# Performance work log

Hardware: AMD Instinct MI355X
Metric: run time of the kernel (lower is better)

The kernel has to match this reference:

```python
import jax, jax.numpy as jnp
import numpy as np

B, S, C = 64, 512, 512   # batch, subseq_length, in_features
H, D = 4, 128            # n_heads, hidden_features (H*D == C)
LN_EPS = 1e-5


def setup_inputs() -> dict:
    key = jax.random.key(0)
    k_h, k_w, k_b = jax.random.split(key, 3)
    h = jax.random.normal(k_h, (B, S, C), dtype=jnp.float32)
    # stacked per-head Linear weights, stored as [H, in, hid] for x @ W
    W = jax.random.normal(k_w, (H, C, D), dtype=jnp.float32) * (1.0 / np.sqrt(C))
    b = jax.random.normal(k_b, (H, D), dtype=jnp.float32) * 0.01
    adj = jnp.ones((S, S), dtype=jnp.float32)
    gamma = jnp.ones((C,), dtype=jnp.float32)
    beta = jnp.zeros((C,), dtype=jnp.float32)
    return {"t": 0, "h": h, "W": W, "b": b, "adj": adj, "gamma": gamma, "beta": beta}


def reference(t, h, W, b, adj, gamma, beta):
    # per-head projection: [H, B, S, D]
    hp = jnp.einsum("bsc,hcd->hbsd", h, W) + b[:, None, None, :]
    # raw scores, multiplicative adjacency mask (non-standard: mask BEFORE softmax by multiply)
    scores = jnp.einsum("hbsd,hbtd->hbst", hp, hp) * adj
    attn = jax.nn.softmax(scores, axis=-1)
    out = jnp.einsum("hbst,hbtd->hbsd", attn, hp)
    # concat heads along feature dim -> [B, S, H*D] == [B, S, C]
    out = jnp.transpose(out, (1, 2, 0, 3)).reshape(h.shape[0], h.shape[1], -1)
    # LayerNorm over last dim
    mu = jnp.mean(out, axis=-1, keepdims=True)
    var = jnp.mean(jnp.square(out - mu), axis=-1, keepdims=True)
    out = (out - mu) * jax.lax.rsqrt(var + LN_EPS) * gamma + beta
    # GELU (exact erf form, matching torch nn.GELU default)
    return jax.nn.gelu(out, approximate=False)
```

## Files before the change

kernel.cpp:

```cpp
#include <hip/hip_runtime.h>
#include <stdint.h>


typedef float  f32x4   __attribute__((ext_vector_type(4)));
typedef short  bf16x8  __attribute__((ext_vector_type(8)));
typedef unsigned short ushort8 __attribute__((ext_vector_type(8)));
typedef unsigned int   uint2v  __attribute__((ext_vector_type(2)));

#define GLD16(src, dst)                                                        \
  __builtin_amdgcn_global_load_lds(                                            \
      (const __attribute__((address_space(1))) void*)(src),                    \
      (__attribute__((address_space(3))) void*)(dst), 16, 0, 0)

__device__ __forceinline__ unsigned short f32_to_bf16(float x) {
  union { float f; unsigned int u; } v; v.f = x;
  unsigned int r = v.u + 0x7FFFu + ((v.u >> 16) & 1u);
  return (unsigned short)(r >> 16);
}
__device__ __forceinline__ float bf16_to_f32(unsigned int h) {
  union { float f; unsigned int u; } v; v.u = h << 16;
  return v.f;
}
__device__ __forceinline__ f32x4 mfma16(bf16x8 a, bf16x8 b, f32x4 c) {
  return __builtin_amdgcn_mfma_f32_16x16x32_bf16(a, b, c, 0, 0, 0);
}
__device__ __forceinline__ float bperm_f(int srcLane, float v) {
  return __int_as_float(__builtin_amdgcn_ds_bpermute(srcLane << 2, __float_as_int(v)));
}
__device__ __forceinline__ uint2v tr_read(const unsigned short* p) {
  uint2v r;
  asm volatile("ds_read_b64_tr_b16 %0, %1"
               : "=v"(r)
               : "v"((const __attribute__((address_space(3))) void*)p)
               : "memory");
  return r;
}

__global__ __launch_bounds__(256) void cast_split_Wt(
    const float* __restrict__ W, unsigned short* __restrict__ whi,
    unsigned short* __restrict__ wlo) {
  int o = blockIdx.x * 256 + threadIdx.x;
  int hd = o >> 16;
  int rem = o & 65535;
  int d = rem >> 9;
  int c = rem & 511;
  float v = W[((size_t)(hd * 512 + c)) * 128 + d];
  unsigned short h0 = f32_to_bf16(v);
  whi[o] = h0;
  wlo[o] = f32_to_bf16(v - bf16_to_f32(h0));
}

__global__ __launch_bounds__(256) void cast_adj(
    const float* __restrict__ src, unsigned short* __restrict__ dst) {
  size_t i = ((size_t)blockIdx.x * 256 + threadIdx.x) * 8;
  f32x4 a = *(const f32x4*)(src + i);
  f32x4 b = *(const f32x4*)(src + i + 4);
  ushort8 o;
#pragma unroll
  for (int e = 0; e < 4; ++e) {
    o[e] = f32_to_bf16(a[e]);
    o[4 + e] = f32_to_bf16(b[e]);
  }
  *(ushort8*)(dst + i) = o;
}

__global__ __launch_bounds__(256, 2) void proj_gemm(
    const float* __restrict__ hsrc,
    const unsigned short* __restrict__ whi, const unsigned short* __restrict__ wlo,
    const float* __restrict__ bias, unsigned short* __restrict__ hp_hi,
    unsigned short* __restrict__ hp_lo) {
  int bid = blockIdx.x;
  int swz = (bid & 7) * 128 + (bid >> 3);
  int nt = swz & 3, mt = swz >> 2;
  int m0 = mt * 128, n0 = nt * 128;

  __shared__ alignas(16) unsigned short Ah[4096], Al[4096], Bh[4096], Bl[4096];

  int tid = threadIdx.x, wv = tid >> 6, lane = tid & 63;
  int l15 = lane & 15, l4 = lane >> 4;
  int wr = wv >> 1, wc = wv & 1;
  int arow = tid >> 3;
  int acol = (tid & 7) * 4;

  f32x4 acc[4][4];
#pragma unroll
  for (int a = 0; a < 4; ++a)
#pragma unroll
    for (int b = 0; b < 4; ++b) acc[a][b] = (f32x4){0.f, 0.f, 0.f, 0.f};

  for (int ks = 0; ks < 16; ++ks) {
    int k0 = ks * 32;
    for (int i = wv; i < 16; i += 4) {
      int grp = i >> 3, j = i & 7;
      int row = j * 16 + (lane >> 2);
      int off = (lane & 3) * 16;
      int sw = ((row >> 1) & 3) << 4;
      const unsigned short* sb = grp ? wlo : whi;
      unsigned short* db = grp ? Bl : Bh;
      GLD16((const char*)sb + ((size_t)(nt * 128 + row) * 512 + k0) * 2 + (off ^ sw),
            db + j * 512);
    }
#pragma unroll
    for (int j = 0; j < 4; ++j) {
      int r = j * 32 + arow;
      f32x4 x = *(const f32x4*)(hsrc + (size_t)(m0 + r) * 512 + k0 + acol);
      unsigned ua = __float_as_uint(x[0]), ub = __float_as_uint(x[1]);
      unsigned uc = __float_as_uint(x[2]), ud = __float_as_uint(x[3]);
      uint2 ph, pl;
      ph.x = (ua >> 16) | (ub & 0xFFFF0000u);
      ph.y = (uc >> 16) | (ud & 0xFFFF0000u);
      float ra = x[0] - __uint_as_float(ua & 0xFFFF0000u);
      float rb = x[1] - __uint_as_float(ub & 0xFFFF0000u);
      float rc = x[2] - __uint_as_float(uc & 0xFFFF0000u);
      float rd = x[3] - __uint_as_float(ud & 0xFFFF0000u);
      pl.x = (__float_as_uint(ra) >> 16) | (__float_as_uint(rb) & 0xFFFF0000u);
      pl.y = (__float_as_uint(rc) >> 16) | (__float_as_uint(rd) & 0xFFFF0000u);
      int boff = r * 64 + ((acol * 2) ^ (((r >> 1) & 3) << 4));
      *(uint2*)((char*)Ah + boff) = ph;
      *(uint2*)((char*)Al + boff) = pl;
    }
    __syncthreads();

    bf16x8 fah[4], fal[4], fbh[4], fbl[4];
#pragma unroll
    for (int f = 0; f < 4; ++f) {
      int mr = wr * 64 + f * 16 + l15;
      int aadr = mr * 64 + ((16 * l4) ^ (((mr >> 1) & 3) << 4));
      fah[f] = *(const bf16x8*)((const char*)Ah + aadr);
      fal[f] = *(const bf16x8*)((const char*)Al + aadr);
      int nr = wc * 64 + f * 16 + l15;
      int badr = nr * 64 + ((16 * l4) ^ (((nr >> 1) & 3) << 4));
      fbh[f] = *(const bf16x8*)((const char*)Bh + badr);
      fbl[f] = *(const bf16x8*)((const char*)Bl + badr);
    }
#pragma unroll
    for (int a = 0; a < 4; ++a)
#pragma unroll
      for (int b = 0; b < 4; ++b) {
        acc[a][b] = mfma16(fah[a], fbh[b], acc[a][b]);
        acc[a][b] = mfma16(fah[a], fbl[b], acc[a][b]);
        acc[a][b] = mfma16(fal[a], fbh[b], acc[a][b]);
      }
    __syncthreads();
  }

#pragma unroll
  for (int a = 0; a < 4; ++a) {
    __syncthreads();
#pragma unroll
    for (int b = 0; b < 4; ++b) {
      int cloc = wc * 64 + b * 16 + l15;
      float bv = bias[n0 + cloc];
#pragma unroll
      for (int r = 0; r < 4; ++r) {
        int rloc = wr * 16 + 4 * l4 + r;
        float v = acc[a][b][r] + bv;
        unsigned short hh = f32_to_bf16(v);
        Ah[rloc * 128 + cloc] = hh;
        Al[rloc * 128 + cloc] = f32_to_bf16(v - bf16_to_f32(hh));
      }
    }
    __syncthreads();
    int rr = tid >> 3, c16 = (tid & 7) * 16;
    int mg = m0 + (rr >> 4) * 64 + a * 16 + (rr & 15);
    bf16x8 vh0 = *(const bf16x8*)(Ah + rr * 128 + c16);
    bf16x8 vh1 = *(const bf16x8*)(Ah + rr * 128 + c16 + 8);
    bf16x8 vl0 = *(const bf16x8*)(Al + rr * 128 + c16);
    bf16x8 vl1 = *(const bf16x8*)(Al + rr * 128 + c16 + 8);
    *(bf16x8*)(hp_hi + (size_t)mg * 512 + n0 + c16) = vh0;
    *(bf16x8*)(hp_hi + (size_t)mg * 512 + n0 + c16 + 8) = vh1;
    *(bf16x8*)(hp_lo + (size_t)mg * 512 + n0 + c16) = vl0;
    *(bf16x8*)(hp_lo + (size_t)mg * 512 + n0 + c16 + 8) = vl1;
  }
}

__global__ __launch_bounds__(256, 3) void attn_kernel(
    const unsigned short* __restrict__ hp_hi, const unsigned short* __restrict__ hp_lo,
    const unsigned short* __restrict__ adjb, unsigned short* __restrict__ ob) {
  int bid = blockIdx.x;
  int swz = (bid & 7) * 256 + (bid >> 3);
  int qt = swz & 7;
  int hd = (swz >> 3) & 3;
  int bb = swz >> 5;
  int q0 = qt * 64;

  __shared__ alignas(16) unsigned short SM[24576];

  int tid = threadIdx.x, w = tid >> 6, lane = tid & 63;
  int l15 = lane & 15, l4 = lane >> 4;
  int qg = q0 + w * 16 + l15;

  bf16x8 qh[4], ql[4];
  {
    size_t base = ((size_t)bb * 512 + qg) * 512 + hd * 128 + 8 * l4;
#pragma unroll
    for (int ds = 0; ds < 4; ++ds) {
      qh[ds] = *(const bf16x8*)(hp_hi + base + ds * 32);
      ql[ds] = *(const bf16x8*)(hp_lo + base + ds * 32);
    }
  }

  f32x4 o[8];
#pragma unroll
  for (int vf = 0; vf < 8; ++vf) o[vf] = (f32x4){0.f, 0.f, 0.f, 0.f};
  float m_run = -3.0e38f, l_run = 0.f;

  const unsigned short* ssb = (w & 2) ? hp_lo : hp_hi;
  int sdst = (w & 2) ? 4096 : 0;
  int sdbase = (w & 1) * 4;
  int skv = lane >> 1, sdh = lane & 1;

  {
    size_t rowb = ((size_t)(bb * 512 + skv)) * 1024 + hd * 256 + sdh * 16;
#pragma unroll
    for (int s2 = 0; s2 < 4; ++s2) {
      int sd = sdbase + s2;
      GLD16((const char*)ssb + rowb + sd * 32, SM + sdst + sd * 512);
    }
  }
  asm volatile("s_waitcnt vmcnt(0)" ::: "memory");
  __syncthreads();

  for (int t = 0; t < 16; ++t) {
    int kv0 = t * 32;
    const unsigned short* Kb = SM + ((t & 1) << 13);
    const unsigned short* Khi = Kb;
    const unsigned short* Klo = Kb + 4096;

    if (t < 15) {
      unsigned short* Nb = SM + (((t + 1) & 1) << 13) + sdst;
      size_t rowb = ((size_t)(bb * 512 + kv0 + 32 + skv)) * 1024 + hd * 256 + sdh * 16;
#pragma unroll
      for (int s2 = 0; s2 < 4; ++s2) {
        int sd = sdbase + s2;
        GLD16((const char*)ssb + rowb + sd * 32, Nb + sd * 512);
      }
    }
    uint2 ua0 = *(const uint2*)(adjb + (size_t)qg * 512 + kv0 + 4 * l4);
    uint2 ua1 = *(const uint2*)(adjb + (size_t)qg * 512 + kv0 + 16 + 4 * l4);
    f32x4 av0, av1;
    av0[0] = bf16_to_f32(ua0.x & 0xFFFFu); av0[1] = bf16_to_f32(ua0.x >> 16);
    av0[2] = bf16_to_f32(ua0.y & 0xFFFFu); av0[3] = bf16_to_f32(ua0.y >> 16);
    av1[0] = bf16_to_f32(ua1.x & 0xFFFFu); av1[1] = bf16_to_f32(ua1.x >> 16);
    av1[2] = bf16_to_f32(ua1.y & 0xFFFFu); av1[3] = bf16_to_f32(ua1.y >> 16);

    f32x4 sc0 = {0.f, 0.f, 0.f, 0.f}, sc1 = {0.f, 0.f, 0.f, 0.f};
#pragma unroll
    for (int ds = 0; ds < 4; ++ds) {
      int boff = (2 * ds + (l4 >> 1)) * 1024 + 16 * (l4 & 1);
      int a0 = boff + l15 * 32;
      int a1 = boff + (16 + l15) * 32;
      bf16x8 kh0 = *(const bf16x8*)((const char*)Khi + a0);
      bf16x8 kl0 = *(const bf16x8*)((const char*)Klo + a0);
      bf16x8 kh1 = *(const bf16x8*)((const char*)Khi + a1);
      bf16x8 kl1 = *(const bf16x8*)((const char*)Klo + a1);
      sc0 = mfma16(kh0, qh[ds], sc0); sc1 = mfma16(kh1, qh[ds], sc1);
      sc0 = mfma16(kh0, ql[ds], sc0); sc1 = mfma16(kh1, ql[ds], sc1);
      sc0 = mfma16(kl0, qh[ds], sc0); sc1 = mfma16(kl1, qh[ds], sc1);
    }

    float p0[4], p1[4];
    float tm = -3.0e38f;
#pragma unroll
    for (int r = 0; r < 4; ++r) {
      p0[r] = sc0[r] * av0[r];
      p1[r] = sc1[r] * av1[r];
      tm = fmaxf(tm, fmaxf(p0[r], p1[r]));
    }
    tm = fmaxf(tm, __shfl_xor(tm, 16));
    tm = fmaxf(tm, __shfl_xor(tm, 32));
    if (__any(tm > m_run + 8.0f)) {
      float mn = fmaxf(m_run, tm);
      float scl = __expf(m_run - mn);
      m_run = mn;
      l_run *= scl;
      f32x4 s4;
#pragma unroll
      for (int r = 0; r < 4; ++r) s4[r] = bperm_f(4 * l4 + r, scl);
#pragma unroll
      for (int vf = 0; vf < 8; ++vf)
#pragma unroll
        for (int r = 0; r < 4; ++r) o[vf][r] *= s4[r];
    }
    float ps = 0.f;
#pragma unroll
    for (int r = 0; r < 4; ++r) {
      p0[r] = __expf(p0[r] - m_run); ps += p0[r];
      p1[r] = __expf(p1[r] - m_run); ps += p1[r];
    }
    ps += __shfl_xor(ps, 16);
    ps += __shfl_xor(ps, 32);
    l_run += ps;

    union PU { bf16x8 v; unsigned u[4]; } pah;
#pragma unroll
    for (int i = 0; i < 4; ++i) {
      float fa = (i < 2) ? p0[2 * i] : p1[2 * (i - 2)];
      float fb = (i < 2) ? p0[2 * i + 1] : p1[2 * (i - 2) + 1];
      pah.u[i] = (__float_as_uint(fa) >> 16) |
                 (__float_as_uint(fb) & 0xFFFF0000u);
    }

    const unsigned short* trb = Khi + lane * 4;
    union VU { bf16x8 v; uint2v u2[2]; } vh[8];
#pragma unroll
    for (int vf = 0; vf < 8; ++vf) {
      vh[vf].u2[0] = tr_read(trb + vf * 512);
      vh[vf].u2[1] = tr_read(trb + vf * 512 + 256);
    }
    asm volatile("s_waitcnt lgkmcnt(0)" ::: "memory");
    __builtin_amdgcn_sched_barrier(0);
#pragma unroll
    for (int vf = 0; vf < 8; ++vf)
      o[vf] = mfma16(pah.v, vh[vf].v, o[vf]);
    asm volatile("s_waitcnt vmcnt(0) lgkmcnt(0)" ::: "memory");
    __syncthreads();
  }

  float rinv = 1.0f / l_run;
  f32x4 r4;
#pragma unroll
  for (int r = 0; r < 4; ++r) r4[r] = bperm_f(4 * l4 + r, rinv);
  float* wbase = (float*)SM + w * 2048;
#pragma unroll
  for (int vf = 0; vf < 8; ++vf)
#pragma unroll
    for (int r = 0; r < 4; ++r)
      wbase[(4 * l4 + r) * 128 + vf * 16 + l15] = o[vf][r] * r4[r];
  __syncthreads();
#pragma unroll
  for (int p = 0; p < 4; ++p) {
    int row = p * 4 + l4;
    f32x4 v0 = *(const f32x4*)(wbase + row * 128 + l15 * 8);
    f32x4 v1 = *(const f32x4*)(wbase + row * 128 + l15 * 8 + 4);
    ushort8 o8;
#pragma unroll
    for (int e = 0; e < 4; ++e) {
      o8[e] = f32_to_bf16(v0[e]);
      o8[4 + e] = f32_to_bf16(v1[e]);
    }
    size_t mg = (size_t)bb * 512 + q0 + w * 16 + row;
    *(ushort8*)(ob + mg * 512 + hd * 128 + l15 * 8) = o8;
  }
}

__global__ __launch_bounds__(256) void ln_gelu_kernel(
    const unsigned short* __restrict__ in, float* __restrict__ outp,
    const float* __restrict__ gamma, const float* __restrict__ beta) {
  int w = threadIdx.x >> 6, lane = threadIdx.x & 63;
  size_t row = (size_t)blockIdx.x * 4 + w;
  ushort8 v = *(const ushort8*)(in + row * 512 + lane * 8);
  float x[8];
#pragma unroll
  for (int e = 0; e < 8; ++e) x[e] = bf16_to_f32((unsigned int)(unsigned short)v[e]);
  float s = 0.f;
#pragma unroll
  for (int e = 0; e < 8; ++e) s += x[e];
#pragma unroll
  for (int off = 32; off >= 1; off >>= 1) s += __shfl_xor(s, off);
  float mu = s * (1.0f / 512.0f);
  float vs = 0.f;
#pragma unroll
  for (int e = 0; e < 8; ++e) {
    float d = x[e] - mu; vs += d * d;
  }
#pragma unroll
  for (int off = 32; off >= 1; off >>= 1) vs += __shfl_xor(vs, off);
  float rs = rsqrtf(vs * (1.0f / 512.0f) + 1e-5f);
  f32x4 g0 = *(const f32x4*)(gamma + lane * 8);
  f32x4 g1 = *(const f32x4*)(gamma + lane * 8 + 4);
  f32x4 b0 = *(const f32x4*)(beta + lane * 8);
  f32x4 b1 = *(const f32x4*)(beta + lane * 8 + 4);
  f32x4 y0, y1;
#pragma unroll
  for (int e = 0; e < 4; ++e) {
    float y = (x[e] - mu) * rs * g0[e] + b0[e];
    y0[e] = 0.5f * y * (1.0f + erff(y * 0.70710678118654752f));
    float z = (x[4 + e] - mu) * rs * g1[e] + b1[e];
    y1[e] = 0.5f * z * (1.0f + erff(z * 0.70710678118654752f));
  }
  float* p = outp + row * 512 + lane * 8;
  *(f32x4*)p = y0;
  *(f32x4*)(p + 4) = y1;
}

extern "C" void kernel_launch(void* const* d_in, const int* in_sizes, int n_in,
                              void* d_out, int out_size, void* d_ws, size_t ws_size,
                              hipStream_t stream) {
  const float* h     = (const float*)d_in[1];
  const float* W     = (const float*)d_in[2];
  const float* bias  = (const float*)d_in[3];
  const float* adj   = (const float*)d_in[4];
  const float* gamma = (const float*)d_in[5];
  const float* beta  = (const float*)d_in[6];
  float* out = (float*)d_out;

  unsigned short* ws = (unsigned short*)d_ws;
  unsigned short* adj_bf = ws;
  unsigned short* ob     = ws + 16777216;
  unsigned short* hp_hi  = ws + 33554432;
  unsigned short* hp_lo  = ws + 50331648;
  unsigned short* Wt_hi  = ws + 67108864;
  unsigned short* Wt_lo  = ws + 67371008;

  cast_split_Wt<<<1024, 256, 0, stream>>>(W, Wt_hi, Wt_lo);
  cast_adj<<<128, 256, 0, stream>>>(adj, adj_bf);
  proj_gemm<<<1024, 256, 0, stream>>>(h, Wt_hi, Wt_lo, bias, hp_hi, hp_lo);
  attn_kernel<<<2048, 256, 0, stream>>>(hp_hi, hp_lo, adj_bf, ob);
  ln_gelu_kernel<<<8192, 256, 0, stream>>>(ob, out, gamma, beta);
}
```

Before: 194.0 us.

## Process two query fragments per wave to reuse K/V tiles in attention

Each attention block now covers 128 query rows instead of 64, and each wave handles two 16-row query fragments that share the same K/V LDS loads and transposed V reads. The aim is to halve K/V global-to-LDS traffic and LDS reads per query, giving more MFMA work per load. In exchange it doubles per-wave accumulators and registers, lowers occupancy (launch bounds 3 to 2), and halves the grid to 1024 blocks, which may leave fewer waves to hide latency.

```diff
diff --git a/kernel.cpp b/kernel.cpp
--- a/kernel.cpp
+++ b/kernel.cpp
@@ -174,36 +174,40 @@
   }
 }
 
-__global__ __launch_bounds__(256, 3) void attn_kernel(
+__global__ __launch_bounds__(256, 2) void attn_kernel(
     const unsigned short* __restrict__ hp_hi, const unsigned short* __restrict__ hp_lo,
     const unsigned short* __restrict__ adjb, unsigned short* __restrict__ ob) {
   int bid = blockIdx.x;
-  int swz = (bid & 7) * 256 + (bid >> 3);
-  int qt = swz & 7;
-  int hd = (swz >> 3) & 3;
-  int bb = swz >> 5;
-  int q0 = qt * 64;
-
-  __shared__ alignas(16) unsigned short SM[24576];
+  int swz = (bid & 7) * 128 + (bid >> 3);
+  int qt = swz & 3;
+  int hd = (swz >> 2) & 3;
+  int bb = swz >> 4;
+  int q0 = qt * 128;
+
+  __shared__ alignas(16) unsigned short SM[28672];
 
   int tid = threadIdx.x, w = tid >> 6, lane = tid & 63;
   int l15 = lane & 15, l4 = lane >> 4;
-  int qg = q0 + w * 16 + l15;
-
-  bf16x8 qh[4], ql[4];
-  {
-    size_t base = ((size_t)bb * 512 + qg) * 512 + hd * 128 + 8 * l4;
+  int qgb = q0 + w * 32 + l15;
+
+  bf16x8 qh[2][4], ql[2][4];
+#pragma unroll
+  for (int nf = 0; nf < 2; ++nf) {
+    size_t base = ((size_t)bb * 512 + qgb + nf * 16) * 512 + hd * 128 + 8 * l4;
 #pragma unroll
     for (int ds = 0; ds < 4; ++ds) {
-      qh[ds] = *(const bf16x8*)(hp_hi + base + ds * 32);
-      ql[ds] = *(const bf16x8*)(hp_lo + base + ds * 32);
-    }
-  }
-
-  f32x4 o[8];
-#pragma unroll
-  for (int vf = 0; vf < 8; ++vf) o[vf] = (f32x4){0.f, 0.f, 0.f, 0.f};
-  float m_run = -3.0e38f, l_run = 0.f;
+      qh[nf][ds] = *(const bf16x8*)(hp_hi + base + ds * 32);
+      ql[nf][ds] = *(const bf16x8*)(hp_lo + base + ds * 32);
+    }
+  }
+
+  f32x4 o[2][8];
+#pragma unroll
+  for (int nf = 0; nf < 2; ++nf)
+#pragma unroll
+    for (int vf = 0; vf < 8; ++vf) o[nf][vf] = (f32x4){0.f, 0.f, 0.f, 0.f};
+  float m_run[2] = {-3.0e38f, -3.0e38f};
+  float l_run[2] = {0.f, 0.f};
 
   const unsigned short* ssb = (w & 2) ? hp_lo : hp_hi;
   int sdst = (w & 2) ? 4096 : 0;
@@ -236,15 +240,19 @@
         GLD16((const char*)ssb + rowb + sd * 32, Nb + sd * 512);
       }
     }
-    uint2 ua0 = *(const uint2*)(adjb + (size_t)qg * 512 + kv0 + 4 * l4);
-    uint2 ua1 = *(const uint2*)(adjb + (size_t)qg * 512 + kv0 + 16 + 4 * l4);
-    f32x4 av0, av1;
-    av0[0] = bf16_to_f32(ua0.x & 0xFFFFu); av0[1] = bf16_to_f32(ua0.x >> 16);
-    av0[2] = bf16_to_f32(ua0.y & 0xFFFFu); av0[3] = bf16_to_f32(ua0.y >> 16);
-    av1[0] = bf16_to_f32(ua1.x & 0xFFFFu); av1[1] = bf16_to_f32(ua1.x >> 16);
-    av1[2] = bf16_to_f32(ua1.y & 0xFFFFu); av1[3] = bf16_to_f32(ua1.y >> 16);
-
-    f32x4 sc0 = {0.f, 0.f, 0.f, 0.f}, sc1 = {0.f, 0.f, 0.f, 0.f};
+    uint2 ua[2][2];
+#pragma unroll
+    for (int nf = 0; nf < 2; ++nf) {
+      const unsigned short* ab = adjb + (size_t)(qgb + nf * 16) * 512 + kv0;
+      ua[nf][0] = *(const uint2*)(ab + 4 * l4);
+      ua[nf][1] = *(const uint2*)(ab + 16 + 4 * l4);
+    }
+
+    f32x4 sc[2][2];
+#pragma unroll
+    for (int nf = 0; nf < 2; ++nf)
+#pragma unroll
+      for (int mf = 0; mf < 2; ++mf) sc[nf][mf] = (f32x4){0.f, 0.f, 0.f, 0.f};
 #pragma unroll
     for (int ds = 0; ds < 4; ++ds) {
       int boff = (2 * ds + (l4 >> 1)) * 1024 + 16 * (l4 & 1);
@@ -254,51 +262,68 @@
       bf16x8 kl0 = *(const bf16x8*)((const char*)Klo + a0);
       bf16x8 kh1 = *(const bf16x8*)((const char*)Khi + a1);
       bf16x8 kl1 = *(const bf16x8*)((const char*)Klo + a1);
-      sc0 = mfma16(kh0, qh[ds], sc0); sc1 = mfma16(kh1, qh[ds], sc1);
-      sc0 = mfma16(kh0, ql[ds], sc0); sc1 = mfma16(kh1, ql[ds], sc1);
-      sc0 = mfma16(kl0, qh[ds], sc0); sc1 = mfma16(kl1, qh[ds], sc1);
-    }
-
-    float p0[4], p1[4];
-    float tm = -3.0e38f;
-#pragma unroll
-    for (int r = 0; r < 4; ++r) {
-      p0[r] = sc0[r] * av0[r];
-      p1[r] = sc1[r] * av1[r];
-      tm = fmaxf(tm, fmaxf(p0[r], p1[r]));
-    }
-    tm = fmaxf(tm, __shfl_xor(tm, 16));
-    tm = fmaxf(tm, __shfl_xor(tm, 32));
-    if (__any(tm > m_run + 8.0f)) {
-      float mn = fmaxf(m_run, tm);
-      float scl = __expf(m_run - mn);
-      m_run = mn;
-      l_run *= scl;
-      f32x4 s4;
-#pragma unroll
-      for (int r = 0; r < 4; ++r) s4[r] = bperm_f(4 * l4 + r, scl);
-#pragma unroll
-      for (int vf = 0; vf < 8; ++vf)
-#pragma unroll
-        for (int r = 0; r < 4; ++r) o[vf][r] *= s4[r];
-    }
-    float ps = 0.f;
-#pragma unroll
-    for (int r = 0; r < 4; ++r) {
-      p0[r] = __expf(p0[r] - m_run); ps += p0[r];
-      p1[r] = __expf(p1[r] - m_run); ps += p1[r];
-    }
-    ps += __shfl_xor(ps, 16);
-    ps += __shfl_xor(ps, 32);
-    l_run += ps;
-
-    union PU { bf16x8 v; unsigned u[4]; } pah;
-#pragma unroll
-    for (int i = 0; i < 4; ++i) {
-      float fa = (i < 2) ? p0[2 * i] : p1[2 * (i - 2)];
-      float fb = (i < 2) ? p0[2 * i + 1] : p1[2 * (i - 2) + 1];
-      pah.u[i] = (__float_as_uint(fa) >> 16) |
-                 (__float_as_uint(fb) & 0xFFFF0000u);
+#pragma unroll
+      for (int nf = 0; nf < 2; ++nf) {
+        sc[nf][0] = mfma16(kh0, qh[nf][ds], sc[nf][0]);
+        sc[nf][1] = mfma16(kh1, qh[nf][ds], sc[nf][1]);
+        sc[nf][0] = mfma16(kh0, ql[nf][ds], sc[nf][0]);
+        sc[nf][1] = mfma16(kh1, ql[nf][ds], sc[nf][1]);
+        sc[nf][0] = mfma16(kl0, qh[nf][ds], sc[nf][0]);
+        sc[nf][1] = mfma16(kl1, qh[nf][ds], sc[nf][1]);
+      }
+    }
+
+    union PU { bf16x8 v; unsigned u[4]; } pah[2];
+#pragma unroll
+    for (int nf = 0; nf < 2; ++nf) {
+      f32x4 av0, av1;
+      av0[0] = bf16_to_f32(ua[nf][0].x & 0xFFFFu);
+      av0[1] = bf16_to_f32(ua[nf][0].x >> 16);
+      av0[2] = bf16_to_f32(ua[nf][0].y & 0xFFFFu);
+      av0[3] = bf16_to_f32(ua[nf][0].y >> 16);
+      av1[0] = bf16_to_f32(ua[nf][1].x & 0xFFFFu);
+      av1[1] = bf16_to_f32(ua[nf][1].x >> 16);
+      av1[2] = bf16_to_f32(ua[nf][1].y & 0xFFFFu);
+      av1[3] = bf16_to_f32(ua[nf][1].y >> 16);
+      float p0[4], p1[4];
+      float tm = -3.0e38f;
+#pragma unroll
+      for (int r = 0; r < 4; ++r) {
+        p0[r] = sc[nf][0][r] * av0[r];
+        p1[r] = sc[nf][1][r] * av1[r];
+        tm = fmaxf(tm, fmaxf(p0[r], p1[r]));
+      }
+      tm = fmaxf(tm, __shfl_xor(tm, 16));
+      tm = fmaxf(tm, __shfl_xor(tm, 32));
+      if (__any(tm > m_run[nf] + 8.0f)) {
+        float mn = fmaxf(m_run[nf], tm);
+        float scl = __expf(m_run[nf] - mn);
+        m_run[nf] = mn;
+        l_run[nf] *= scl;
+        f32x4 s4;
+#pragma unroll
+        for (int r = 0; r < 4; ++r) s4[r] = bperm_f(4 * l4 + r, scl);
+#pragma unroll
+        for (int vf = 0; vf < 8; ++vf)
+#pragma unroll
+          for (int r = 0; r < 4; ++r) o[nf][vf][r] *= s4[r];
+      }
+      float ps = 0.f;
+#pragma unroll
+      for (int r = 0; r < 4; ++r) {
+        p0[r] = __expf(p0[r] - m_run[nf]); ps += p0[r];
+        p1[r] = __expf(p1[r] - m_run[nf]); ps += p1[r];
+      }
+      ps += __shfl_xor(ps, 16);
+      ps += __shfl_xor(ps, 32);
+      l_run[nf] += ps;
+#pragma unroll
+      for (int i = 0; i < 4; ++i) {
+        float fa = (i < 2) ? p0[2 * i] : p1[2 * (i - 2)];
+        float fb = (i < 2) ? p0[2 * i + 1] : p1[2 * (i - 2) + 1];
+        pah[nf].u[i] = (__float_as_uint(fa) >> 16) |
+                       (__float_as_uint(fb) & 0xFFFF0000u);
+      }
     }
 
     const unsigned short* trb = Khi + lane * 4;
@@ -311,36 +336,42 @@
     asm volatile("s_waitcnt lgkmcnt(0)" ::: "memory");
     __builtin_amdgcn_sched_barrier(0);
 #pragma unroll
+    for (int vf = 0; vf < 8; ++vf) {
+      o[0][vf] = mfma16(pah[0].v, vh[vf].v, o[0][vf]);
+      o[1][vf] = mfma16(pah[1].v, vh[vf].v, o[1][vf]);
+    }
+    asm volatile("s_waitcnt vmcnt(0) lgkmcnt(0)" ::: "memory");
+    __syncthreads();
+  }
+
+#pragma unroll
+  for (int nf = 0; nf < 2; ++nf) {
+    float rinv = 1.0f / l_run[nf];
+    f32x4 r4;
+#pragma unroll
+    for (int r = 0; r < 4; ++r) r4[r] = bperm_f(4 * l4 + r, rinv);
+    float* wbase = (float*)SM + w * 2048;
+#pragma unroll
     for (int vf = 0; vf < 8; ++vf)
-      o[vf] = mfma16(pah.v, vh[vf].v, o[vf]);
-    asm volatile("s_waitcnt vmcnt(0) lgkmcnt(0)" ::: "memory");
-    __syncthreads();
-  }
-
-  float rinv = 1.0f / l_run;
-  f32x4 r4;
-#pragma unroll
-  for (int r = 0; r < 4; ++r) r4[r] = bperm_f(4 * l4 + r, rinv);
-  float* wbase = (float*)SM + w * 2048;
-#pragma unroll
-  for (int vf = 0; vf < 8; ++vf)
-#pragma unroll
-    for (int r = 0; r < 4; ++r)
-      wbase[(4 * l4 + r) * 128 + vf * 16 + l15] = o[vf][r] * r4[r];
-  __syncthreads();
-#pragma unroll
-  for (int p = 0; p < 4; ++p) {
-    int row = p * 4 + l4;
-    f32x4 v0 = *(const f32x4*)(wbase + row * 128 + l15 * 8);
-    f32x4 v1 = *(const f32x4*)(wbase + row * 128 + l15 * 8 + 4);
-    ushort8 o8;
-#pragma unroll
-    for (int e = 0; e < 4; ++e) {
-      o8[e] = f32_to_bf16(v0[e]);
-      o8[4 + e] = f32_to_bf16(v1[e]);
-    }
-    size_t mg = (size_t)bb * 512 + q0 + w * 16 + row;
-    *(ushort8*)(ob + mg * 512 + hd * 128 + l15 * 8) = o8;
+#pragma unroll
+      for (int r = 0; r < 4; ++r)
+        wbase[(4 * l4 + r) * 128 + vf * 16 + l15] = o[nf][vf][r] * r4[r];
+    __syncthreads();
+#pragma unroll
+    for (int p = 0; p < 4; ++p) {
+      int row = p * 4 + l4;
+      f32x4 v0 = *(const f32x4*)(wbase + row * 128 + l15 * 8);
+      f32x4 v1 = *(const f32x4*)(wbase + row * 128 + l15 * 8 + 4);
+      ushort8 o8;
+#pragma unroll
+      for (int e = 0; e < 4; ++e) {
+        o8[e] = f32_to_bf16(v0[e]);
+        o8[4 + e] = f32_to_bf16(v1[e]);
+      }
+      size_t mg = (size_t)bb * 512 + q0 + w * 32 + nf * 16 + row;
+      *(ushort8*)(ob + mg * 512 + hd * 128 + l15 * 8) = o8;
+    }
+    __syncthreads();
   }
 }
 
@@ -406,6 +437,6 @@
   cast_split_Wt<<<1024, 256, 0, stream>>>(W, Wt_hi, Wt_lo);
   cast_adj<<<128, 256, 0, stream>>>(adj, adj_bf);
   proj_gemm<<<1024, 256, 0, stream>>>(h, Wt_hi, Wt_lo, bias, hp_hi, hp_lo);
-  attn_kernel<<<2048, 256, 0, stream>>>(hp_hi, hp_lo, adj_bf, ob);
+  attn_kernel<<<1024, 256, 0, stream>>>(hp_hi, hp_lo, adj_bf, ob);
   ln_gelu_kernel<<<8192, 256, 0, stream>>>(ob, out, gamma, beta);
 }
```

After: 187.2 us. 3.5% less time.
